# Optimization experiments

Measured on AMD Instinct MI355X. Metric: run time of the kernel, lower is better.

The kernel has to match this reference:

```python
import jax, jax.numpy as jnp
import numpy as np

B, N, D = 64, 1024, 1024

def setup_inputs() -> dict:
    key = jax.random.key(0)
    k1, k2, k3, k4, k5 = jax.random.split(key, 5)
    s = 1.0 / np.sqrt(D)
    return {
        "h_t": jax.random.normal(k1, (B, D), dtype=jnp.float32),
        "keys": jax.random.normal(k2, (B, N, D), dtype=jnp.float32),
        "W_h": jax.random.uniform(k3, (D, D), jnp.float32, -s, s),
        "W_k": jax.random.uniform(k4, (D, D), jnp.float32, -s, s),
        "v": jax.random.uniform(k5, (D,), jnp.float32, -s, s),
    }

def reference(h_t, keys, W_h, W_k, v):
    # W_h(h_t): [B, D]; W_k(keys): [B, N, D]  (nn.Linear computes x @ W.T)
    qh = h_t @ W_h.T                       # [B, D]
    kh = jnp.einsum('bnd,ed->bne', keys, W_k)  # [B, N, D]
    energy = jnp.tanh(qh[:, None, :] + kh)     # [B, N, D]
    scores = jnp.einsum('bnd,d->bn', energy, v)  # [B, N]
    alpha = jax.nn.softmax(scores, axis=-1)      # [B, N]
    context = jnp.einsum('bn,bnd->bd', alpha, keys)  # [B, D]
    return (context, alpha)
```

## Files before the change

### kernel.cpp

```cpp
#include <hip/hip_runtime.h>
#include <math.h>

#define BB 64
#define NN 1024
#define DD 1024

typedef __bf16 bf16x8 __attribute__((ext_vector_type(8)));
typedef _Float16 f16x8 __attribute__((ext_vector_type(8)));
typedef float f32x4 __attribute__((ext_vector_type(4)));
typedef unsigned short u16x8 __attribute__((ext_vector_type(8)));

#define GLOAD_LDS16(g, l)                                                  \
    __builtin_amdgcn_global_load_lds(                                      \
        (const __attribute__((address_space(1))) unsigned int*)(g),        \
        (__attribute__((address_space(3))) unsigned int*)(l), 16, 0, 0)

__device__ __forceinline__ float fast_tanh(float x) {
    return 1.f - 2.f / (__expf(2.f * x) + 1.f);
}


__global__ __launch_bounds__(256) void k_cvt(const float* __restrict__ keys,
                                             const float* __restrict__ W_k,
                                             _Float16* __restrict__ keysT,
                                             _Float16* __restrict__ wkT) {
    const int nt = blockIdx.x;
    const int bb = blockIdx.y;
    const int ks = blockIdx.z;
    const int t = threadIdx.x;
    const float* src = (bb == 64) ? (W_k + (size_t)nt * 128 * DD)
                                  : (keys + ((size_t)bb * NN + nt * 128) * DD);
    _Float16* dst = (bb == 64) ? (wkT + (size_t)nt * 32 * 4096)
                               : (keysT + (((size_t)bb * 8 + nt) * 32) * 4096);
    const int p0 = t * 8;
    const int n0 = p0 >> 5;
    const int k0 = p0 & 31;
    const int ksw = (k0 >> 3) ^ ((n0 >> 1) & 3);
    for (int kt = ks * 8; kt < ks * 8 + 8; ++kt) {
#pragma unroll
        for (int r = 0; r < 2; ++r) {
            const int n = n0 + r * 64;
            const float4* s4 = (const float4*)(src + (size_t)n * DD + kt * 32 + k0);
            float4 a = s4[0], b4 = s4[1];
            f16x8 h = {(_Float16)a.x,  (_Float16)a.y,  (_Float16)a.z,  (_Float16)a.w,
                       (_Float16)b4.x, (_Float16)b4.y, (_Float16)b4.z, (_Float16)b4.w};
            *(f16x8*)(dst + (size_t)kt * 4096 + n * 32 + ksw * 8) = h;
        }
    }
}

__global__ __launch_bounds__(256) void k_qh(const float* __restrict__ h_t,
                                            const float* __restrict__ W_h,
                                            float* __restrict__ qh,
                                            float* __restrict__ scores) {
    __shared__ float hs[DD];
    __shared__ float red2[128];
    const int b = blockIdx.x;
    const int et = blockIdx.y;
    const int t = threadIdx.x;
    if (t < 128) scores[b * NN + et * 128 + t] = 0.f;
    ((float4*)hs)[t] = ((const float4*)(h_t + (size_t)b * DD))[t];
    __syncthreads();
    const int el = t & 127;
    const int half = t >> 7;
    const int e = et * 128 + el;
    const float4* wrow = (const float4*)(W_h + (size_t)e * DD) + half * 128;
    const float* hp = hs + half * 512;
    float acc = 0.f;
#pragma unroll 4
    for (int k4 = 0; k4 < 128; ++k4) {
        float4 wv = wrow[k4];
        acc = fmaf(wv.x, hp[4 * k4 + 0], acc);
        acc = fmaf(wv.y, hp[4 * k4 + 1], acc);
        acc = fmaf(wv.z, hp[4 * k4 + 2], acc);
        acc = fmaf(wv.w, hp[4 * k4 + 3], acc);
    }
    if (half == 1) red2[el] = acc;
    __syncthreads();
    if (half == 0) qh[(size_t)b * DD + e] = acc + red2[el];
}

#define PHASE(KT, SLAB, VM)                                                   \
    do {                                                                      \
        const _Float16* ab = As + ((KT) & 3) * 8192 + aofs;                   \
        const _Float16* bb2 = Bs + ((KT) & 3) * 8192 + bofs;                  \
        f16x8 af[8], bf[4];                                                   \
        _Pragma("unroll") for (int mi = 0; mi < 8; ++mi)                      \
            af[mi] = *(const f16x8*)(ab + mi * 512);                          \
        _Pragma("unroll") for (int ni = 0; ni < 4; ++ni)                      \
            bf[ni] = *(const f16x8*)(bb2 + ni * 512);                         \
        if ((SLAB) < 32) {                                                    \
            const size_t go = (size_t)(SLAB) * 8192;                          \
            const int sl = (SLAB) & 3;                                        \
            GLOAD_LDS16(a0 + go, AsB + sl * 16384 + tid * 16);                \
            GLOAD_LDS16(a1 + go, AsB + sl * 16384 + 8192 + tid * 16);         \
            GLOAD_LDS16(b0 + go, BsB + sl * 16384 + tid * 16);                \
            GLOAD_LDS16(b1 + go, BsB + sl * 16384 + 8192 + tid * 16);         \
        }                                                                     \
        asm volatile("s_waitcnt lgkmcnt(0)" ::: "memory");                    \
        __builtin_amdgcn_sched_barrier(0);                                    \
        __builtin_amdgcn_s_setprio(1);                                        \
        _Pragma("unroll") for (int mi = 0; mi < 8; ++mi)                      \
            _Pragma("unroll") for (int ni = 0; ni < 4; ++ni)                  \
                acc[mi][ni] = __builtin_amdgcn_mfma_f32_16x16x32_f16(         \
                    af[mi], bf[ni], acc[mi][ni], 0, 0, 0);                    \
        __builtin_amdgcn_s_setprio(0);                                        \
        asm volatile(VM ::: "memory");                                        \
        __builtin_amdgcn_s_barrier();                                         \
        __builtin_amdgcn_sched_barrier(0);                                    \
    } while (0)

__global__ __launch_bounds__(512, 2) void k_sc(const _Float16* __restrict__ keysT,
                                               const _Float16* __restrict__ wkT,
                                               const float* __restrict__ v,
                                               const float* __restrict__ qh,
                                               float* __restrict__ scores) {
    __shared__ _Float16 As[4 * 8192];
    __shared__ _Float16 Bs[4 * 8192];
    __shared__ float vs[256];
    __shared__ float qs[256];
    __shared__ float red[256][4];

    const int tid = threadIdx.x;
    const int gid = blockIdx.x;
    const int wg = (gid & 7) * 128 + (gid >> 3);
    const int b = wg >> 4;
    const int x = wg & 15;
    const int tn = x >> 2;
    const int te = x & 3;

    if (tid < 256) {
        vs[tid] = v[te * 256 + tid];
        qs[tid] = qh[b * DD + te * 256 + tid];
    }

    const char* a0 = (const char*)(keysT + (((size_t)b * 8 + tn * 2) * 32) * 4096) + tid * 16;
    const char* a1 = a0 + 32 * 8192;
    const char* b0 = (const char*)(wkT + (((size_t)te * 2) * 32) * 4096) + tid * 16;
    const char* b1 = b0 + 32 * 8192;
    char* AsB = (char*)As;
    char* BsB = (char*)Bs;

    const int w = tid >> 6, lane = tid & 63;
    const int wm = w & 1, wn = w >> 1;
    const int lcol = lane & 15, quad = lane >> 4;
    const int qx = quad ^ ((lcol >> 1) & 3);
    const int aofs = wm * 4096 + lcol * 32 + qx * 8;
    const int bofs = (wn >> 1) * 4096 + (wn & 1) * 2048 + lcol * 32 + qx * 8;

    f32x4 acc[8][4];
#pragma unroll
    for (int mi = 0; mi < 8; ++mi)
#pragma unroll
        for (int ni = 0; ni < 4; ++ni) acc[mi][ni] = (f32x4){0.f, 0.f, 0.f, 0.f};

#pragma unroll
    for (int s = 0; s < 3; ++s) {
        const size_t go = (size_t)s * 8192;
        GLOAD_LDS16(a0 + go, AsB + s * 16384 + tid * 16);
        GLOAD_LDS16(a1 + go, AsB + s * 16384 + 8192 + tid * 16);
        GLOAD_LDS16(b0 + go, BsB + s * 16384 + tid * 16);
        GLOAD_LDS16(b1 + go, BsB + s * 16384 + 8192 + tid * 16);
    }
    asm volatile("s_waitcnt vmcnt(8)" ::: "memory");
    __builtin_amdgcn_s_barrier();
    __builtin_amdgcn_sched_barrier(0);

#pragma unroll 1
    for (int kt = 0; kt < 29; ++kt) {
        PHASE(kt, kt + 3, "s_waitcnt vmcnt(8)");
    }
    PHASE(29, 32, "s_waitcnt vmcnt(4)");
    PHASE(30, 32, "s_waitcnt vmcnt(0)");
    PHASE(31, 32, "");

    float part[8][4];
#pragma unroll
    for (int mi = 0; mi < 8; ++mi)
#pragma unroll
        for (int r = 0; r < 4; ++r) part[mi][r] = 0.f;
#pragma unroll
    for (int mi = 0; mi < 8; ++mi)
#pragma unroll
        for (int ni = 0; ni < 4; ++ni) {
            const int e = wn * 64 + ni * 16 + lcol;
            const float vv = vs[e];
            const float qv = qs[e];
#pragma unroll
            for (int r = 0; r < 4; ++r)
                part[mi][r] += vv * fast_tanh(qv + acc[mi][ni][r]);
        }
#pragma unroll
    for (int mi = 0; mi < 8; ++mi)
#pragma unroll
        for (int r = 0; r < 4; ++r) {
            float p = part[mi][r];
            p += __shfl_xor(p, 1);
            p += __shfl_xor(p, 2);
            p += __shfl_xor(p, 4);
            p += __shfl_xor(p, 8);
            if (lcol == 0) red[wm * 128 + mi * 16 + quad * 4 + r][wn] = p;
        }
    __syncthreads();
    if (tid < 256)
        atomicAdd(&scores[b * NN + tn * 256 + tid],
                  red[tid][0] + red[tid][1] + red[tid][2] + red[tid][3]);
}

__global__ __launch_bounds__(256) void k_sm(const float* __restrict__ scores,
                                            float* __restrict__ alpha) {
    const int b = blockIdx.x;
    const int t = threadIdx.x;
    float x[4];
    float m = -1e30f;
#pragma unroll
    for (int j = 0; j < 4; ++j) {
        x[j] = scores[b * NN + t + 256 * j];
        m = fmaxf(m, x[j]);
    }
#pragma unroll
    for (int mask = 32; mask >= 1; mask >>= 1) m = fmaxf(m, __shfl_xor(m, mask));
    __shared__ float wred[4];
    __shared__ float wsum[4];
    const int wv = t >> 6;
    if ((t & 63) == 0) wred[wv] = m;
    __syncthreads();
    m = fmaxf(fmaxf(wred[0], wred[1]), fmaxf(wred[2], wred[3]));
    float s = 0.f;
#pragma unroll
    for (int j = 0; j < 4; ++j) {
        x[j] = expf(x[j] - m);
        s += x[j];
    }
#pragma unroll
    for (int mask = 32; mask >= 1; mask >>= 1) s += __shfl_xor(s, mask);
    if ((t & 63) == 0) wsum[wv] = s;
    __syncthreads();
    s = wsum[0] + wsum[1] + wsum[2] + wsum[3];
    const float inv = 1.f / s;
#pragma unroll
    for (int j = 0; j < 4; ++j) alpha[b * NN + t + 256 * j] = x[j] * inv;
}

__global__ __launch_bounds__(256) void k_ctx(const _Float16* __restrict__ keysT,
                                             const float* __restrict__ alpha,
                                             float* __restrict__ context) {
    __shared__ float al[NN];
    __shared__ float red[64][33];
    const int kt = blockIdx.x;
    const int b = blockIdx.y;
    const int t = threadIdx.x;
#pragma unroll
    for (int j = 0; j < 4; ++j) al[t + 256 * j] = alpha[b * NN + t + 256 * j];
    __syncthreads();

    const int p0 = t * 8;
    const int g = t >> 2;
    const int q = t & 3;
    const int qe = q ^ ((g >> 1) & 3);
    float acc[8];
#pragma unroll
    for (int j = 0; j < 8; ++j) acc[j] = 0.f;

    for (int nt = 0; nt < 8; ++nt) {
        const _Float16* base = keysT + (((size_t)b * 8 + nt) * 32 + kt) * 4096;
#pragma unroll
        for (int r = 0; r < 2; ++r) {
            f16x8 kv = *(const f16x8*)(base + r * 2048 + p0);
            const float a = al[nt * 128 + r * 64 + g];
#pragma unroll
            for (int j = 0; j < 8; ++j) acc[j] = fmaf(a, (float)kv[j], acc[j]);
        }
    }
#pragma unroll
    for (int j = 0; j < 8; ++j) red[g][qe * 8 + j] = acc[j];
    __syncthreads();
    if (t < 32) {
        float s = 0.f;
#pragma unroll 8
        for (int n = 0; n < 64; ++n) s += red[n][t];
        context[(size_t)b * DD + kt * 32 + t] = s;
    }
}

__global__ __launch_bounds__(256) void qh_fb(const float* __restrict__ h_t,
                                             const float* __restrict__ W_h,
                                             float* __restrict__ qh,
                                             float* __restrict__ scores) {
    __shared__ float hs[DD];
    const int b = blockIdx.y;
    const int e = blockIdx.x * 256 + threadIdx.x;
    scores[(blockIdx.y * 4 + blockIdx.x) * 256 + threadIdx.x] = 0.f;
    for (int i = threadIdx.x; i < DD; i += 256) hs[i] = h_t[b * DD + i];
    __syncthreads();
    const float4* wrow = (const float4*)(W_h + (size_t)e * DD);
    float acc = 0.f;
#pragma unroll 4
    for (int k4 = 0; k4 < DD / 4; ++k4) {
        float4 w = wrow[k4];
        acc = fmaf(w.x, hs[4 * k4 + 0], acc);
        acc = fmaf(w.y, hs[4 * k4 + 1], acc);
        acc = fmaf(w.z, hs[4 * k4 + 2], acc);
        acc = fmaf(w.w, hs[4 * k4 + 3], acc);
    }
    qh[b * DD + e] = acc;
}

#define SPAD 40
__device__ __forceinline__ void split16(const float4* __restrict__ src,
                                        unsigned short* hi, unsigned short* lo) {
    float x[16];
    float4 v0 = src[0], v1 = src[1], v2 = src[2], v3 = src[3];
    x[0] = v0.x; x[1] = v0.y; x[2] = v0.z; x[3] = v0.w;
    x[4] = v1.x; x[5] = v1.y; x[6] = v1.z; x[7] = v1.w;
    x[8] = v2.x; x[9] = v2.y; x[10] = v2.z; x[11] = v2.w;
    x[12] = v3.x; x[13] = v3.y; x[14] = v3.z; x[15] = v3.w;
#pragma unroll
    for (int i = 0; i < 16; ++i) {
        unsigned int u = __float_as_uint(x[i]);
        hi[i] = (unsigned short)(u >> 16);
        float hif = __uint_as_float(u & 0xFFFF0000u);
        float lof = x[i] - hif;
        lo[i] = (unsigned short)(__float_as_uint(lof) >> 16);
    }
}

__global__ __launch_bounds__(256, 2) void scores_fb(const float* __restrict__ keys,
                                                    const float* __restrict__ W_k,
                                                    const float* __restrict__ v,
                                                    const float* __restrict__ qh,
                                                    float* __restrict__ scores) {
    __shared__ unsigned short Ah[128 * SPAD];
    __shared__ unsigned short Al[128 * SPAD];
    __shared__ unsigned short Bh[128 * SPAD];
    __shared__ unsigned short Bl[128 * SPAD];
    __shared__ float vs[128];
    __shared__ float qs[128];
    __shared__ float red[128][2];

    const int tid = threadIdx.x;
    const int cp = blockIdx.x;
    const int rt = blockIdx.y;
    const int b = rt >> 3;
    const int n0 = (rt & 7) * 128;
    const int e0 = cp * 128;
    if (tid < 128) {
        vs[tid] = v[e0 + tid];
        qs[tid] = qh[b * DD + e0 + tid];
    }
    const float* Ag = keys + ((size_t)b * NN + n0) * DD;
    const float* Bg = W_k + (size_t)e0 * DD;
    const int w = tid >> 6;
    const int lane = tid & 63;
    const int wm = w & 1;
    const int we = w >> 1;
    const int lcol = lane & 15;
    const int quad = lane >> 4;
    f32x4 acc[4][4];
#pragma unroll
    for (int mi = 0; mi < 4; ++mi)
#pragma unroll
        for (int ni = 0; ni < 4; ++ni) acc[mi][ni] = (f32x4){0.f, 0.f, 0.f, 0.f};
    const int srow = tid >> 1;
    const int sseg = tid & 1;
    float4 pa[4], pb[4];
    {
        const float4* as = (const float4*)(Ag + (size_t)srow * DD + sseg * 16);
        const float4* bs = (const float4*)(Bg + (size_t)srow * DD + sseg * 16);
#pragma unroll
        for (int i = 0; i < 4; ++i) { pa[i] = as[i]; pb[i] = bs[i]; }
    }
    for (int kt = 0; kt < DD / 32; ++kt) {
        __syncthreads();
        {
            unsigned short hi[16], lo[16];
            split16(pa, hi, lo);
            u16x8* dh = (u16x8*)&Ah[srow * SPAD + sseg * 16];
            u16x8* dl = (u16x8*)&Al[srow * SPAD + sseg * 16];
            dh[0] = *(u16x8*)&hi[0]; dh[1] = *(u16x8*)&hi[8];
            dl[0] = *(u16x8*)&lo[0]; dl[1] = *(u16x8*)&lo[8];
            split16(pb, hi, lo);
            u16x8* eh = (u16x8*)&Bh[srow * SPAD + sseg * 16];
            u16x8* el = (u16x8*)&Bl[srow * SPAD + sseg * 16];
            eh[0] = *(u16x8*)&hi[0]; eh[1] = *(u16x8*)&hi[8];
            el[0] = *(u16x8*)&lo[0]; el[1] = *(u16x8*)&lo[8];
        }
        if (kt + 1 < DD / 32) {
            const int k0 = (kt + 1) * 32;
            const float4* as = (const float4*)(Ag + (size_t)srow * DD + k0 + sseg * 16);
            const float4* bs = (const float4*)(Bg + (size_t)srow * DD + k0 + sseg * 16);
#pragma unroll
            for (int i = 0; i < 4; ++i) { pa[i] = as[i]; pb[i] = bs[i]; }
        }
        __syncthreads();
        bf16x8 ah[4], al2[4], bh[4], bl2[4];
#pragma unroll
        for (int mi = 0; mi < 4; ++mi) {
            const int r = wm * 64 + mi * 16 + lcol;
            ah[mi] = *(const bf16x8*)&Ah[r * SPAD + quad * 8];
            al2[mi] = *(const bf16x8*)&Al[r * SPAD + quad * 8];
        }
#pragma unroll
        for (int ni = 0; ni < 4; ++ni) {
            const int r = we * 64 + ni * 16 + lcol;
            bh[ni] = *(const bf16x8*)&Bh[r * SPAD + quad * 8];
            bl2[ni] = *(const bf16x8*)&Bl[r * SPAD + quad * 8];
        }
#pragma unroll
        for (int mi = 0; mi < 4; ++mi)
#pragma unroll
            for (int ni = 0; ni < 4; ++ni) {
                acc[mi][ni] = __builtin_amdgcn_mfma_f32_16x16x32_bf16(ah[mi], bh[ni], acc[mi][ni], 0, 0, 0);
                acc[mi][ni] = __builtin_amdgcn_mfma_f32_16x16x32_bf16(ah[mi], bl2[ni], acc[mi][ni], 0, 0, 0);
                acc[mi][ni] = __builtin_amdgcn_mfma_f32_16x16x32_bf16(al2[mi], bh[ni], acc[mi][ni], 0, 0, 0);
            }
    }
    float part[4][4];
#pragma unroll
    for (int mi = 0; mi < 4; ++mi)
#pragma unroll
        for (int r = 0; r < 4; ++r) part[mi][r] = 0.f;
#pragma unroll
    for (int mi = 0; mi < 4; ++mi)
#pragma unroll
        for (int ni = 0; ni < 4; ++ni) {
            const int e = we * 64 + ni * 16 + lcol;
            const float vv = vs[e];
            const float qv = qs[e];
#pragma unroll
            for (int r = 0; r < 4; ++r)
                part[mi][r] += vv * fast_tanh(qv + acc[mi][ni][r]);
        }
#pragma unroll
    for (int mi = 0; mi < 4; ++mi)
#pragma unroll
        for (int r = 0; r < 4; ++r) {
            float p = part[mi][r];
            p += __shfl_xor(p, 1);
            p += __shfl_xor(p, 2);
            p += __shfl_xor(p, 4);
            p += __shfl_xor(p, 8);
            if (lcol == 0) red[wm * 64 + mi * 16 + quad * 4 + r][we] = p;
        }
    __syncthreads();
    if (tid < 128) atomicAdd(&scores[b * NN + n0 + tid], red[tid][0] + red[tid][1]);
}

__global__ __launch_bounds__(256) void sm_fb(const float* __restrict__ scores,
                                             float* __restrict__ alpha,
                                             float* __restrict__ context) {
    const int b = blockIdx.x;
    const int t = threadIdx.x;
#pragma unroll
    for (int j = 0; j < 4; ++j) context[b * DD + t + 256 * j] = 0.f;
    float x[4];
    float m = -1e30f;
#pragma unroll
    for (int j = 0; j < 4; ++j) {
        x[j] = scores[b * NN + t + 256 * j];
        m = fmaxf(m, x[j]);
    }
#pragma unroll
    for (int mask = 32; mask >= 1; mask >>= 1) m = fmaxf(m, __shfl_xor(m, mask));
    __shared__ float wred[4];
    __shared__ float wsum[4];
    const int wv = t >> 6;
    if ((t & 63) == 0) wred[wv] = m;
    __syncthreads();
    m = fmaxf(fmaxf(wred[0], wred[1]), fmaxf(wred[2], wred[3]));
    float s = 0.f;
#pragma unroll
    for (int j = 0; j < 4; ++j) {
        x[j] = expf(x[j] - m);
        s += x[j];
    }
#pragma unroll
    for (int mask = 32; mask >= 1; mask >>= 1) s += __shfl_xor(s, mask);
    if ((t & 63) == 0) wsum[wv] = s;
    __syncthreads();
    s = wsum[0] + wsum[1] + wsum[2] + wsum[3];
    const float inv = 1.f / s;
#pragma unroll
    for (int j = 0; j < 4; ++j) alpha[b * NN + t + 256 * j] = x[j] * inv;
}

__global__ __launch_bounds__(256) void ctx_fb(const float* __restrict__ keys,
                                              const float* __restrict__ alpha,
                                              float* __restrict__ context) {
    const int b = blockIdx.y;
    const int nc = blockIdx.x;
    const int t = threadIdx.x;
    __shared__ float al[64];
    if (t < 64) al[t] = alpha[b * NN + nc * 64 + t];
    __syncthreads();
    const float4* kp = (const float4*)(keys + ((size_t)b * NN + nc * 64) * DD);
    float4 acc = {0.f, 0.f, 0.f, 0.f};
#pragma unroll 4
    for (int n = 0; n < 64; ++n) {
        const float a = al[n];
        float4 kv = kp[(size_t)n * (DD / 4) + t];
        acc.x = fmaf(a, kv.x, acc.x);
        acc.y = fmaf(a, kv.y, acc.y);
        acc.z = fmaf(a, kv.z, acc.z);
        acc.w = fmaf(a, kv.w, acc.w);
    }
    float* cp = context + b * DD + 4 * t;
    atomicAdd(cp + 0, acc.x);
    atomicAdd(cp + 1, acc.y);
    atomicAdd(cp + 2, acc.z);
    atomicAdd(cp + 3, acc.w);
}

extern "C" void kernel_launch(void* const* d_in, const int* in_sizes, int n_in,
                              void* d_out, int out_size, void* d_ws, size_t ws_size,
                              hipStream_t stream) {
    const float* h_t = (const float*)d_in[0];
    const float* keys = (const float*)d_in[1];
    const float* W_h = (const float*)d_in[2];
    const float* W_k = (const float*)d_in[3];
    const float* v = (const float*)d_in[4];

    float* context = (float*)d_out;
    float* alpha = (float*)d_out + BB * DD;
    float* qh = (float*)d_ws;
    float* scores = (float*)d_ws + BB * DD;

    const size_t wkT_off = (size_t)2 * BB * DD * sizeof(float);
    const size_t keysT_off = wkT_off + (size_t)DD * DD * 2;
    const size_t need = keysT_off + (size_t)BB * NN * DD * 2;

    if (ws_size >= need) {
        _Float16* wkT = (_Float16*)((char*)d_ws + wkT_off);
        _Float16* keysT = (_Float16*)((char*)d_ws + keysT_off);
        k_cvt<<<dim3(8, 65, 4), 256, 0, stream>>>(keys, W_k, keysT, wkT);
        k_qh<<<dim3(64, 8), 256, 0, stream>>>(h_t, W_h, qh, scores);
        k_sc<<<dim3(1024), 512, 0, stream>>>(keysT, wkT, v, qh, scores);
        k_sm<<<BB, 256, 0, stream>>>(scores, alpha);
        k_ctx<<<dim3(32, 64), 256, 0, stream>>>(keysT, alpha, context);
    } else {
        qh_fb<<<dim3(4, BB), 256, 0, stream>>>(h_t, W_h, qh, scores);
        scores_fb<<<dim3(8, 512), 256, 0, stream>>>(keys, W_k, v, qh, scores);
        sm_fb<<<BB, 256, 0, stream>>>(scores, alpha, context);
        ctx_fb<<<dim3(16, BB), 256, 0, stream>>>(keys, alpha, context);
    }
}
```

Before: 609.7 us.

## Restructure score GEMM pipeline into half-tile phases with double-buffered stages

Reorganizes the k_sc main loop so each k-slab is split into two M-halves per phase. B fragments are reused across both halves and fewer A fragments stay live at once. The LDS layout changes from four single-slab buffers to two double-slab buffers, and global-to-LDS loads are interleaved at a finer granularity with the wait moved to the start of each phase. The aim is to cut register pressure and smooth load/compute overlap, at the cost of more barriers per k-step and more intricate vmcnt bookkeeping.

```diff
diff --git a/kernel.cpp b/kernel.cpp
--- a/kernel.cpp
+++ b/kernel.cpp
@@ -80,33 +80,42 @@
     if (half == 0) qh[(size_t)b * DD + e] = acc + red2[el];
 }
 
-#define PHASE(KT, SLAB, VM)                                                   \
+#define NOSTG do { } while (0)
+
+#define STG2(APAN, BPAN, T, KT, SL, C)                                        \
     do {                                                                      \
-        const _Float16* ab = As + ((KT) & 3) * 8192 + aofs;                   \
-        const _Float16* bb2 = Bs + ((KT) & 3) * 8192 + bofs;                  \
-        f16x8 af[8], bf[4];                                                   \
-        _Pragma("unroll") for (int mi = 0; mi < 8; ++mi)                      \
-            af[mi] = *(const f16x8*)(ab + mi * 512);                          \
-        _Pragma("unroll") for (int ni = 0; ni < 4; ++ni)                      \
-            bf[ni] = *(const f16x8*)(bb2 + ni * 512);                         \
-        if ((SLAB) < 32) {                                                    \
-            const size_t go = (size_t)(SLAB) * 8192;                          \
-            const int sl = (SLAB) & 3;                                        \
-            GLOAD_LDS16(a0 + go, AsB + sl * 16384 + tid * 16);                \
-            GLOAD_LDS16(a1 + go, AsB + sl * 16384 + 8192 + tid * 16);         \
-            GLOAD_LDS16(b0 + go, BsB + sl * 16384 + tid * 16);                \
-            GLOAD_LDS16(b1 + go, BsB + sl * 16384 + 8192 + tid * 16);         \
+        const size_t go_ = (size_t)((T) * 2 + (KT)) * 8192;                   \
+        GLOAD_LDS16(APAN + go_, AsB + (SL) * 32768 + (C) * 8192 + tid * 16);  \
+        GLOAD_LDS16(BPAN + go_, BsB + (SL) * 32768 + (C) * 8192 + tid * 16);  \
+    } while (0)
+
+#define PH(SL, KS, MH, LOADB, STG, VMW)                                       \
+    do {                                                                      \
+        if ((VMW) == 8) asm volatile("s_waitcnt vmcnt(8)" ::: "memory");      \
+        else if ((VMW) == 4) asm volatile("s_waitcnt vmcnt(4)" ::: "memory"); \
+        else if ((VMW) == 0) asm volatile("s_waitcnt vmcnt(0)" ::: "memory"); \
+        __builtin_amdgcn_s_barrier();                                         \
+        __builtin_amdgcn_sched_barrier(0);                                    \
+        if (LOADB) {                                                          \
+            _Pragma("unroll") for (int ni = 0; ni < 4; ++ni)                  \
+                bf[ni] = *(const f16x8*)(Bs + (SL) * 16384 +                  \
+                    ((KS) * 2 + beh) * 4096 + (brow + ni * 16) * 32 + qx8);   \
         }                                                                     \
+        f16x8 af[4];                                                          \
+        _Pragma("unroll") for (int mi = 0; mi < 4; ++mi)                      \
+            af[mi] = *(const f16x8*)(As + (SL) * 16384 +                      \
+                ((KS) * 2 + wm) * 4096 +                                      \
+                ((MH) * 64 + mi * 16 + lcol) * 32 + qx8);                     \
+        STG;                                                                  \
         asm volatile("s_waitcnt lgkmcnt(0)" ::: "memory");                    \
         __builtin_amdgcn_sched_barrier(0);                                    \
         __builtin_amdgcn_s_setprio(1);                                        \
-        _Pragma("unroll") for (int mi = 0; mi < 8; ++mi)                      \
+        _Pragma("unroll") for (int mi = 0; mi < 4; ++mi)                      \
             _Pragma("unroll") for (int ni = 0; ni < 4; ++ni)                  \
-                acc[mi][ni] = __builtin_amdgcn_mfma_f32_16x16x32_f16(         \
-                    af[mi], bf[ni], acc[mi][ni], 0, 0, 0);                    \
+                acc[(MH) * 4 + mi][ni] =                                      \
+                    __builtin_amdgcn_mfma_f32_16x16x32_f16(                   \
+                        af[mi], bf[ni], acc[(MH) * 4 + mi][ni], 0, 0, 0);     \
         __builtin_amdgcn_s_setprio(0);                                        \
-        asm volatile(VM ::: "memory");                                        \
-        __builtin_amdgcn_s_barrier();                                         \
         __builtin_amdgcn_sched_barrier(0);                                    \
     } while (0)
 
@@ -115,8 +124,8 @@
                                                const float* __restrict__ v,
                                                const float* __restrict__ qh,
                                                float* __restrict__ scores) {
-    __shared__ _Float16 As[4 * 8192];
-    __shared__ _Float16 Bs[4 * 8192];
+    __shared__ _Float16 As[2 * 16384];
+    __shared__ _Float16 Bs[2 * 16384];
     __shared__ float vs[256];
     __shared__ float qs[256];
     __shared__ float red[256][4];
@@ -134,45 +143,50 @@
         qs[tid] = qh[b * DD + te * 256 + tid];
     }
 
-    const char* a0 = (const char*)(keysT + (((size_t)b * 8 + tn * 2) * 32) * 4096) + tid * 16;
-    const char* a1 = a0 + 32 * 8192;
-    const char* b0 = (const char*)(wkT + (((size_t)te * 2) * 32) * 4096) + tid * 16;
-    const char* b1 = b0 + 32 * 8192;
+    const char* a0 = (const char*)(keysT + (((size_t)b * 8 + tn * 2 + 0) * 32) * 4096) + tid * 16;
+    const char* a1 = (const char*)(keysT + (((size_t)b * 8 + tn * 2 + 1) * 32) * 4096) + tid * 16;
+    const char* b0 = (const char*)(wkT + (((size_t)te * 2 + 0) * 32) * 4096) + tid * 16;
+    const char* b1 = (const char*)(wkT + (((size_t)te * 2 + 1) * 32) * 4096) + tid * 16;
     char* AsB = (char*)As;
     char* BsB = (char*)Bs;
 
     const int w = tid >> 6, lane = tid & 63;
     const int wm = w & 1, wn = w >> 1;
     const int lcol = lane & 15, quad = lane >> 4;
-    const int qx = quad ^ ((lcol >> 1) & 3);
-    const int aofs = wm * 4096 + lcol * 32 + qx * 8;
-    const int bofs = (wn >> 1) * 4096 + (wn & 1) * 2048 + lcol * 32 + qx * 8;
+    const int qx8 = (quad ^ ((lcol >> 1) & 3)) * 8;
+    const int beh = wn >> 1;
+    const int brow = (wn & 1) * 64 + lcol;
 
     f32x4 acc[8][4];
 #pragma unroll
     for (int mi = 0; mi < 8; ++mi)
 #pragma unroll
         for (int ni = 0; ni < 4; ++ni) acc[mi][ni] = (f32x4){0.f, 0.f, 0.f, 0.f};
-
-#pragma unroll
-    for (int s = 0; s < 3; ++s) {
-        const size_t go = (size_t)s * 8192;
-        GLOAD_LDS16(a0 + go, AsB + s * 16384 + tid * 16);
-        GLOAD_LDS16(a1 + go, AsB + s * 16384 + 8192 + tid * 16);
-        GLOAD_LDS16(b0 + go, BsB + s * 16384 + tid * 16);
-        GLOAD_LDS16(b1 + go, BsB + s * 16384 + 8192 + tid * 16);
-    }
-    asm volatile("s_waitcnt vmcnt(8)" ::: "memory");
-    __builtin_amdgcn_s_barrier();
-    __builtin_amdgcn_sched_barrier(0);
+    f16x8 bf[4];
+
+    STG2(a0, b0, 0, 0, 0, 0);
+    STG2(a1, b1, 0, 0, 0, 1);
+    STG2(a0, b0, 0, 1, 0, 2);
+    STG2(a1, b1, 0, 1, 0, 3);
+    STG2(a0, b0, 1, 0, 1, 0);
+    STG2(a1, b1, 1, 0, 1, 1);
 
 #pragma unroll 1
-    for (int kt = 0; kt < 29; ++kt) {
-        PHASE(kt, kt + 3, "s_waitcnt vmcnt(8)");
-    }
-    PHASE(29, 32, "s_waitcnt vmcnt(4)");
-    PHASE(30, 32, "s_waitcnt vmcnt(0)");
-    PHASE(31, 32, "");
+    for (int t = 0; t < 14; ++t) {
+        const int s = t & 1, s1 = s ^ 1;
+        PH(s, 0, 0, 1, STG2(a0, b0, t + 1, 1, s1, 2), 8);
+        PH(s, 0, 1, 0, STG2(a1, b1, t + 1, 1, s1, 3), -1);
+        PH(s, 1, 0, 1, STG2(a0, b0, t + 2, 0, s, 0), 8);
+        PH(s, 1, 1, 0, STG2(a1, b1, t + 2, 0, s, 1), -1);
+    }
+    PH(0, 0, 0, 1, STG2(a0, b0, 15, 1, 1, 2), 8);
+    PH(0, 0, 1, 0, STG2(a1, b1, 15, 1, 1, 3), -1);
+    PH(0, 1, 0, 1, NOSTG, 8);
+    PH(0, 1, 1, 0, NOSTG, -1);
+    PH(1, 0, 0, 1, NOSTG, 4);
+    PH(1, 0, 1, 0, NOSTG, -1);
+    PH(1, 1, 0, 1, NOSTG, 0);
+    PH(1, 1, 1, 0, NOSTG, -1);
 
     float part[8][4];
 #pragma unroll
```

New measurement: 623.2 us. 2.2% more time.
